# Kernel tuning notes

Hardware: AMD Instinct MI355X
Metric: run time of the kernel (lower is better)

The kernel has to match this reference:

```python
import jax, jax.numpy as jnp
import numpy as np

B, C, H, W = 1, 256, 512, 512
DS = 4
HD, WD = H // DS, W // DS
N_NOISE = 32
N_CLUSTERS = 8


def setup_inputs() -> dict:
    key = jax.random.key(0)
    k1, k2, k3, k4, k5 = jax.random.split(key, 5)
    x = jax.random.normal(k1, (B, C, H, W), dtype=jnp.float32)
    # deterministic 'HDBSCAN' labels over the B*C=256 channel-tokens:
    # first 224 channels in 8 clusters of 28, last 32 channels are noise (-1)
    n_clustered = C - N_NOISE
    labels_np = np.concatenate([
        np.arange(n_clustered) % N_CLUSTERS,
        -np.ones(N_NOISE, dtype=np.int64),
    ]).astype(np.int32)
    labels = jnp.asarray(labels_np)
    noise_idx = jnp.arange(n_clustered, C, dtype=jnp.int32)  # channels with label -1
    # grouped 1x1 conv (groups=C, 3 outputs per channel): per-output scalar weight+bias
    w_qkv = jax.random.normal(k2, (3 * C,), dtype=jnp.float32) * 0.02
    b_qkv = jax.random.normal(k3, (3 * C,), dtype=jnp.float32) * 0.02
    # depthwise ConvTranspose2d(kernel=stride=DS, groups=C): per-channel DSxDS kernel
    w_up = jax.random.normal(k4, (C, DS, DS), dtype=jnp.float32) * 0.25
    b_up = jax.random.normal(k5, (C,), dtype=jnp.float32) * 0.02
    return {"x": x, "labels": labels, "noise_idx": noise_idx,
            "w_qkv": w_qkv, "b_qkv": b_qkv, "w_up": w_up, "b_up": b_up}


def _l2norm(a):
    n = jnp.linalg.norm(a, axis=-1, keepdims=True)
    return a / jnp.maximum(n, 1e-12)


def reference(x, labels, noise_idx, w_qkv, b_qkv, w_up, b_up):
    # --- MaxPool2d(DS, DS) ---  (B=1)
    xd = x.reshape(C, HD, DS, WD, DS).max(axis=(2, 4))          # (C, HD, WD)
    xdf = xd.reshape(C, HD * WD)                                 # (C, hw)
    # --- grouped 1x1 qkv conv: out channel o = x[o//3]*w[o]+b[o]; then chunk(3)
    #     reproduces the torch code exactly, incl. its interleaved channel layout ---
    qkv = jnp.repeat(xdf, 3, axis=0) * w_qkv[:, None] + b_qkv[:, None]  # (3C, hw)
    q, k, v = qkv[:C], qkv[C:2 * C], qkv[2 * C:]
    # --- per-cluster attention as a single masked softmax over C tokens ---
    valid = labels != -1
    same = (labels[:, None] == labels[None, :]) & valid[:, None] & valid[None, :]
    scores = q @ k.T                                             # (C, C), no scaling (as in source)
    scores = jnp.where(same, scores, jnp.finfo(scores.dtype).min)
    attn = jax.nn.softmax(scores, axis=-1)
    attn = jnp.where(valid[:, None], attn, 0.0)                  # noise rows -> 0 output
    out_ds = attn @ v                                            # (C, hw)
    # --- depthwise ConvTranspose2d, stride==kernel -> non-overlapping blocks ---
    out_sp = out_ds.reshape(C, HD, WD)
    up = jnp.einsum('chw,cab->chawb', out_sp, w_up).reshape(C, H, W)
    up = (up + b_up[:, None, None])[None]                        # (1, C, H, W)
    # --- noise features & cosine similarity ---
    nf = x.reshape(B, C, H * W)[:, noise_idx, :]                 # (B, n_noise, HW)
    cf = up.reshape(B, C, H * W)                                 # (B, C, HW)
    sim = jnp.einsum('bch,bnh->bcn', _l2norm(cf), _l2norm(nf)).mean(axis=-1)  # (B, C)
    similar = sim.reshape(B, C, 1, 1)
    out = up + (1.0 - similar) * x
    return out, nf.reshape(B, N_NOISE, H, W)
```

## Files before the change

### kernel.cpp

```cpp
#include <hip/hip_runtime.h>
#include <math.h>

#define C_ 256
#define H_ 512
#define W_ 512
#define HW_ (H_*W_)
#define HD_ 128
#define WD_ 128
#define P_ (HD_*WD_)
#define NN_ 32
#define GR_ 86
#define NSL_ 128

#define XD_OFF     0ull
#define SDS_OFF    4194304ull
#define GT_OFF     8388608ull
#define GPART_OFF  8650752ull
#define DSTP_OFF   8650752ull
#define S_OFF      9641984ull
#define SPART_OFF  9642240ull
#define NSQP_OFF   9650432ull
#define GSUMP_OFF  9651456ull
#define BETA_OFF   9651584ull
#define M_OFF      9651840ull
#define SCALE_OFF  9674368ull

typedef float nfloat4 __attribute__((ext_vector_type(4)));

__device__ __forceinline__ void nt_store4(float4 v, float* p) {
    nfloat4 nv;
    nv.x = v.x; nv.y = v.y; nv.z = v.z; nv.w = v.w;
    __builtin_nontemporal_store(nv, (nfloat4*)p);
}

__device__ __forceinline__ float wsum64(float v) {
#pragma unroll
    for (int off = 32; off > 0; off >>= 1) v += __shfl_down(v, off, 64);
    return v;
}

__global__ void __launch_bounds__(256) k_pre(
        const float* __restrict__ x, const int* __restrict__ nidx,
        float* __restrict__ xd, float* __restrict__ outnf,
        float* __restrict__ Spart, float* __restrict__ nsqp) {
    int b = blockIdx.x;
    int c = b >> 5, seg = b & 31;
    int t = threadIdx.x;
    __shared__ int sn;
    if (t == 0) {
        int nn = -1;
        for (int n = 0; n < NN_; n++)
            if (nidx[n] == c) nn = n;
        sn = nn;
    }
    __syncthreads();
    int n = sn;
    int wd = t & 127;
    int hl = t >> 7;
    float ssum = 0.f, ss = 0.f;
    const float* xc = x + (size_t)c * HW_;
    float* nfc = outnf + (size_t)(n < 0 ? 0 : n) * HW_;
#pragma unroll
    for (int q = 0; q < 2; q++) {
        int hd = 4 * seg + hl + 2 * q;
        const float4* xr = (const float4*)(xc + (size_t)(4 * hd) * W_) + wd;
        float4 r0 = xr[0], r1 = xr[128], r2 = xr[256], r3 = xr[384];
        if (n >= 0) {
            float* nr = nfc + (size_t)(4 * hd) * W_ + 4 * wd;
            nt_store4(r0, nr);
            nt_store4(r1, nr + 512);
            nt_store4(r2, nr + 1024);
            nt_store4(r3, nr + 1536);
            ss += r0.x*r0.x + r0.y*r0.y + r0.z*r0.z + r0.w*r0.w
                + r1.x*r1.x + r1.y*r1.y + r1.z*r1.z + r1.w*r1.w
                + r2.x*r2.x + r2.y*r2.y + r2.z*r2.z + r2.w*r2.w
                + r3.x*r3.x + r3.y*r3.y + r3.z*r3.z + r3.w*r3.w;
        }
        float m0 = fmaxf(fmaxf(r0.x, r0.y), fmaxf(r0.z, r0.w));
        float m1 = fmaxf(fmaxf(r1.x, r1.y), fmaxf(r1.z, r1.w));
        float m2 = fmaxf(fmaxf(r2.x, r2.y), fmaxf(r2.z, r2.w));
        float m3 = fmaxf(fmaxf(r3.x, r3.y), fmaxf(r3.z, r3.w));
        float m = fmaxf(fmaxf(m0, m1), fmaxf(m2, m3));
        xd[(size_t)c * P_ + (size_t)hd * WD_ + wd] = m;
        ssum += m;
    }
    __shared__ float red[4];
    float tt = wsum64(ssum);
    int wid = t >> 6, ln = t & 63;
    if (ln == 0) red[wid] = tt;
    __syncthreads();
    if (t == 0) Spart[c * 32 + seg] = red[0] + red[1] + red[2] + red[3];
    if (n >= 0) {
        __syncthreads();
        float t2 = wsum64(ss);
        if (ln == 0) red[wid] = t2;
        __syncthreads();
        if (t == 0) nsqp[n * 32 + seg] = red[0] + red[1] + red[2] + red[3];
    }
}

__global__ void __launch_bounds__(256) k_mid(
        const float* __restrict__ x, const int* __restrict__ nidx,
        const float* __restrict__ nsqp, const float* __restrict__ Spart,
        const float* __restrict__ xd,
        float* __restrict__ gt, float* __restrict__ gsump,
        float* __restrict__ gpart, float* __restrict__ S) {
    __shared__ float smem[2 * 32 * 132];
    int bid = blockIdx.x;
    int t = threadIdx.x;
    if (bid < 128) {
        float* inv_ = smem;
        int* ncs = (int*)(smem + 32);
        float* red = smem + 64;
        if (t < NN_) {
            const float* np = nsqp + t * 32;
            float s = 0.f;
#pragma unroll
            for (int k = 0; k < 32; k++) s += np[k];
            inv_[t] = (1.f / 32.f) / fmaxf(sqrtf(s), 1e-12f);
            ncs[t] = nidx[t];
        }
        __syncthreads();
        int h = bid;
        int w = t & 127, a0 = t >> 7;
        float acc[2][4] = {{0.f,0.f,0.f,0.f},{0.f,0.f,0.f,0.f}};
#pragma unroll 4
        for (int n = 0; n < NN_; n++) {
            const float* base = x + (size_t)ncs[n] * HW_ + (size_t)(4 * h) * W_ + 4 * w;
            float4 va = *(const float4*)(base + (size_t)a0 * W_);
            float4 vb = *(const float4*)(base + (size_t)(a0 + 2) * W_);
            float iv = inv_[n];
            acc[0][0] += va.x * iv; acc[0][1] += va.y * iv;
            acc[0][2] += va.z * iv; acc[0][3] += va.w * iv;
            acc[1][0] += vb.x * iv; acc[1][1] += vb.y * iv;
            acc[1][2] += vb.z * iv; acc[1][3] += vb.w * iv;
        }
        float gs = 0.f;
#pragma unroll
        for (int q = 0; q < 2; q++) {
            int a = a0 + 2 * q;
#pragma unroll
            for (int bb = 0; bb < 4; bb++) {
                float g = acc[q][bb];
                gt[(size_t)(a * 4 + bb) * P_ + h * WD_ + w] = g;
                gs += g;
            }
        }
        float tt = wsum64(gs);
        int wid = t >> 6, ln = t & 63;
        if (ln == 0) red[wid] = tt;
        __syncthreads();
        if (t == 0) gsump[bid] = red[0] + red[1] + red[2] + red[3];
    } else if (bid < 128 + NSL_) {
        int sl = bid - 128;
        float (*As)[132] = (float(*)[132])smem;
        float (*Bs)[132] = (float(*)[132])(smem + 32 * 132);
        int tx = t & 15, ty = t >> 4;
        int p0 = sl * 128;
        float acc[8][8];
#pragma unroll
        for (int i = 0; i < 8; i++)
#pragma unroll
            for (int j = 0; j < 8; j++) acc[i][j] = 0.f;
        for (int ch = 0; ch < 4; ch++) {
            int pb = p0 + ch * 32;
            __syncthreads();
#pragma unroll
            for (int kk = 0; kk < 16; kk++) {
                int lin = kk * 256 + t;
                int row = lin >> 5;
                int pp = lin & 31;
                float av = 0.f, bv = 0.f;
                if (row < GR_) {
                    av = xd[(size_t)row * P_ + pb + pp];
                    bv = xd[(size_t)(85 + row) * P_ + pb + pp];
                }
                As[pp][row] = av;
                Bs[pp][row] = bv;
            }
            __syncthreads();
            for (int pp = 0; pp < 32; pp++) {
                float4 fa0 = *(const float4*)&As[pp][8 * tx];
                float4 fa1 = *(const float4*)&As[pp][8 * tx + 4];
                float4 fb0 = *(const float4*)&Bs[pp][8 * ty];
                float4 fb1 = *(const float4*)&Bs[pp][8 * ty + 4];
                float fa[8] = {fa0.x, fa0.y, fa0.z, fa0.w, fa1.x, fa1.y, fa1.z, fa1.w};
                float fb[8] = {fb0.x, fb0.y, fb0.z, fb0.w, fb1.x, fb1.y, fb1.z, fb1.w};
#pragma unroll
                for (int ii = 0; ii < 8; ii++)
#pragma unroll
                    for (int jj = 0; jj < 8; jj++) acc[ii][jj] += fa[ii] * fb[jj];
            }
        }
        float* gp = gpart + (size_t)sl * 7744;
#pragma unroll
        for (int ii = 0; ii < 8; ii++) {
            int ga = 8 * tx + ii;
            if (ga < GR_) {
#pragma unroll
                for (int jj = 0; jj < 8; jj++) {
                    int gb = 8 * ty + jj;
                    if (gb < GR_) gp[ga * 88 + gb] = acc[ii][jj];
                }
            }
        }
    } else {
        if (t < C_) {
            const float* sp = Spart + t * 32;
            float s = 0.f;
#pragma unroll
            for (int k = 0; k < 32; k++) s += sp[k];
            S[t] = s;
        }
    }
}

__global__ void __launch_bounds__(256) k_attn(
        const int* __restrict__ labels, const float* __restrict__ wqkv,
        const float* __restrict__ bqkv, const float* __restrict__ gpart,
        const float* __restrict__ S, float* __restrict__ M,
        float* __restrict__ beta) {
    int i = blockIdx.x, j = threadIdx.x;
    __shared__ float grow[GR_];
    __shared__ float Mloc[GR_];
    __shared__ float red[4];
    __shared__ float bc;
    int li = labels[i];
    if (li < 0) {
        if (j < GR_) M[i * 88 + j] = 0.f;
        if (j == 0) beta[i] = 0.f;
        return;
    }
    int a = i / 3;
    if (j < GR_) {
        Mloc[j] = 0.f;
        const float* gp = gpart + (size_t)a * 88 + j;
        float s = 0.f;
#pragma unroll 8
        for (int sl = 0; sl < NSL_; sl++) s += gp[(size_t)sl * 7744];
        grow[j] = s;
    }
    __syncthreads();
    float wq = wqkv[i], bq = bqkv[i];
    int kidx = 256 + j;
    int bk = kidx / 3;
    float wk = wqkv[kidx], bkb = bqkv[kidx];
    int lj = labels[j];
    bool same = (lj == li);
    float score = -3.0e38f;
    if (same)
        score = wq * wk * grow[bk - 85] + wq * bkb * S[a] + bq * wk * S[bk] +
                16384.f * bq * bkb;
    int wid = j >> 6, ln = j & 63;
    float m = score;
#pragma unroll
    for (int off = 32; off > 0; off >>= 1) m = fmaxf(m, __shfl_down(m, off, 64));
    if (ln == 0) red[wid] = m;
    __syncthreads();
    if (j == 0) bc = fmaxf(fmaxf(red[0], red[1]), fmaxf(red[2], red[3]));
    __syncthreads();
    float mx = bc;
    float e = same ? expf(score - mx) : 0.f;
    __syncthreads();
    float t = wsum64(e);
    if (ln == 0) red[wid] = t;
    __syncthreads();
    if (j == 0) bc = red[0] + red[1] + red[2] + red[3];
    __syncthreads();
    float attn = e / bc;
    int vidx = 512 + j;
    int vr = vidx / 3 - 170;
    float wv = wqkv[vidx], bv = bqkv[vidx];
    __syncthreads();
    float bp = wsum64(attn * bv);
    if (ln == 0) red[wid] = bp;
    __syncthreads();
    if (j == 0) beta[i] = red[0] + red[1] + red[2] + red[3];
    atomicAdd(&Mloc[vr], attn * wv);
    __syncthreads();
    if (j < GR_) M[i * 88 + j] = Mloc[j];
}

__global__ void __launch_bounds__(256) k_outds(
        const float* __restrict__ xd, const float* __restrict__ gt,
        const float* __restrict__ M, const float* __restrict__ beta,
        float* __restrict__ sds, float* __restrict__ dstp) {
    __shared__ float Mt[16][88];
    __shared__ float bt[16];
    __shared__ float sdsL[16][258];
    __shared__ float gtsL[16][258];
    int t = threadIdx.x;
    int p0 = blockIdx.x * 256;
    int i0 = blockIdx.y * 16;
    for (int idx = t; idx < 16 * 88; idx += 256)
        Mt[idx / 88][idx % 88] = M[(size_t)(i0 + idx / 88) * 88 + (idx % 88)];
    if (t < 16) bt[t] = beta[i0 + t];
#pragma unroll 4
    for (int ab = 0; ab < 16; ab++)
        gtsL[ab][t] = gt[(size_t)ab * P_ + p0 + t];
    __syncthreads();
    float acc[16];
#pragma unroll
    for (int ii = 0; ii < 16; ii++) acc[ii] = bt[ii];
    const float* xb = xd + (size_t)170 * P_ + p0 + t;
    for (int r = 0; r < 84; r += 4) {
        float x0 = xb[(size_t)r * P_];
        float x1 = xb[(size_t)(r + 1) * P_];
        float x2 = xb[(size_t)(r + 2) * P_];
        float x3 = xb[(size_t)(r + 3) * P_];
#pragma unroll
        for (int ii = 0; ii < 16; ii++) {
            float4 mv = *(const float4*)&Mt[ii][r];
            acc[ii] += mv.x * x0 + mv.y * x1 + mv.z * x2 + mv.w * x3;
        }
    }
    {
        float x0 = xb[(size_t)84 * P_];
        float x1 = xb[(size_t)85 * P_];
#pragma unroll
        for (int ii = 0; ii < 16; ii++)
            acc[ii] += Mt[ii][84] * x0 + Mt[ii][85] * x1;
    }
#pragma unroll
    for (int ii = 0; ii < 16; ii++) {
        sds[(size_t)(i0 + ii) * P_ + p0 + t] = acc[ii];
        sdsL[ii][t] = acc[ii];
    }
    __syncthreads();
    int ch = t & 15, ab = t >> 4;
    bool do1 = (t < 16), do2 = (t >= 16 && t < 32);
    float D = 0.f, sx = 0.f;
    for (int k = 0; k < 256; k++) {
        float sv = sdsL[ch][k];
        float gv = gtsL[ab][k];
        D += sv * gv;
        if (do1) sx += sv;
        if (do2) sx += sv * sv;
    }
    size_t base = ((size_t)(i0 + ch) * 64 + blockIdx.x) * 18;
    dstp[base + ab] = D;
    if (do1) dstp[base + 16] = sx;
    if (do2) dstp[base + 17] = sx;
}

__global__ void __launch_bounds__(64) k_sim(
        const float* __restrict__ dstp, const float* __restrict__ gsump,
        const float* __restrict__ wup, const float* __restrict__ bup,
        float* __restrict__ scale) {
    int c = blockIdx.x, t = threadIdx.x;
    const float* dp = dstp + ((size_t)c * 64 + t) * 18;
    float vals[19];
#pragma unroll
    for (int q = 0; q < 18; q++) vals[q] = dp[q];
    vals[18] = gsump[t] + gsump[t + 64];
#pragma unroll
    for (int q = 0; q < 19; q++) vals[q] = wsum64(vals[q]);
    if (t == 0) {
        float gs = vals[18];
        float wsm = 0.f, wsq = 0.f, dd = 0.f;
#pragma unroll
        for (int ab = 0; ab < 16; ab++) {
            float w = wup[c * 16 + ab];
            wsm += w;
            wsq += w * w;
            dd += w * vals[ab];
        }
        float s1 = vals[16], s2 = vals[17];
        float b = bup[c];
        float dot = dd + b * gs;
        float n2 = wsq * s2 + 2.f * b * wsm * s1 + (float)HW_ * b * b;
        float nrm = sqrtf(fmaxf(n2, 0.f));
        scale[c] = 1.f - dot / fmaxf(nrm, 1e-12f);
    }
}

__global__ void __launch_bounds__(256) k_final(
        const float* __restrict__ x, const float* __restrict__ sds,
        const float* __restrict__ wup, const float* __restrict__ bup,
        const float* __restrict__ scale, float* __restrict__ out) {
    size_t idx = (size_t)blockIdx.x * 256 + threadIdx.x;
    int wq = (int)(idx & 127);
    int y = (int)((idx >> 7) & 511);
    int c = (int)(idx >> 16);
    float sv = sds[(size_t)c * P_ + (size_t)(y >> 2) * WD_ + wq];
    float4 wu = *(const float4*)(wup + c * 16 + (y & 3) * 4);
    float b = bup[c];
    float sc = scale[c];
    float4 xv = ((const float4*)x)[idx];
    float4 o;
    o.x = sv * wu.x + b + sc * xv.x;
    o.y = sv * wu.y + b + sc * xv.y;
    o.z = sv * wu.z + b + sc * xv.z;
    o.w = sv * wu.w + b + sc * xv.w;
    nt_store4(o, out + 4 * idx);
}

extern "C" void kernel_launch(void* const* d_in, const int* in_sizes, int n_in,
                              void* d_out, int out_size, void* d_ws, size_t ws_size,
                              hipStream_t stream) {
    const float* x = (const float*)d_in[0];
    const int* labels = (const int*)d_in[1];
    const int* nidx = (const int*)d_in[2];
    const float* wqkv = (const float*)d_in[3];
    const float* bqkv = (const float*)d_in[4];
    const float* wup = (const float*)d_in[5];
    const float* bup = (const float*)d_in[6];
    float* out = (float*)d_out;
    float* ws = (float*)d_ws;

    float* xd = ws + XD_OFF;
    float* sds = ws + SDS_OFF;
    float* gt = ws + GT_OFF;
    float* gpart = ws + GPART_OFF;
    float* dstp = ws + DSTP_OFF;
    float* S = ws + S_OFF;
    float* Spart = ws + SPART_OFF;
    float* nsqp = ws + NSQP_OFF;
    float* gsump = ws + GSUMP_OFF;
    float* beta = ws + BETA_OFF;
    float* M = ws + M_OFF;
    float* scale = ws + SCALE_OFF;
    float* outnf = out + (size_t)C_ * HW_;

    k_pre<<<C_ * 32, 256, 0, stream>>>(x, nidx, xd, outnf, Spart, nsqp);
    k_mid<<<128 + NSL_ + 1, 256, 0, stream>>>(x, nidx, nsqp, Spart, xd, gt, gsump, gpart, S);
    k_attn<<<256, 256, 0, stream>>>(labels, wqkv, bqkv, gpart, S, M, beta);
    k_outds<<<dim3(64, 16), 256, 0, stream>>>(xd, gt, M, beta, sds, dstp);
    k_sim<<<256, 64, 0, stream>>>(dstp, gsump, wup, bup, scale);
    k_final<<<65536, 256, 0, stream>>>(x, sds, wup, bup, scale, out);
}
```

Before: 210.1 us.

## Split noise-sum blocks 4x across rows and give final kernel two rows per thread

The noise-channel weighted-sum part of k_mid now uses 512 blocks instead of 128. Each block handles one sub-row, with the 32 noise channels split between two thread halves and combined through shared memory. The gsump partials grow to 512 entries and k_sim sums eight per lane; the workspace offsets shift to make room. k_final is restructured so each thread reuses one downsampled value for two output rows, using nontemporal loads of x and half as many blocks. The aim is more parallelism in the mid stage and fewer redundant sds/weight loads in the bandwidth-bound final pass, at the cost of an extra shared-memory reduction.

New measurement: 214.6 us. 1.02x slower.

```diff
diff --git a/kernel.cpp b/kernel.cpp
--- a/kernel.cpp
+++ b/kernel.cpp
@@ -21,9 +21,9 @@
 #define SPART_OFF  9642240ull
 #define NSQP_OFF   9650432ull
 #define GSUMP_OFF  9651456ull
-#define BETA_OFF   9651584ull
-#define M_OFF      9651840ull
-#define SCALE_OFF  9674368ull
+#define BETA_OFF   9651968ull
+#define M_OFF      9652224ull
+#define SCALE_OFF  9674752ull
 
 typedef float nfloat4 __attribute__((ext_vector_type(4)));
 
@@ -31,6 +31,13 @@
     nfloat4 nv;
     nv.x = v.x; nv.y = v.y; nv.z = v.z; nv.w = v.w;
     __builtin_nontemporal_store(nv, (nfloat4*)p);
+}
+
+__device__ __forceinline__ float4 nt_load4(const float* p) {
+    nfloat4 nv = __builtin_nontemporal_load((const nfloat4*)p);
+    float4 v;
+    v.x = nv.x; v.y = nv.y; v.z = nv.z; v.w = nv.w;
+    return v;
 }
 
 __device__ __forceinline__ float wsum64(float v) {
@@ -108,10 +115,11 @@
     __shared__ float smem[2 * 32 * 132];
     int bid = blockIdx.x;
     int t = threadIdx.x;
-    if (bid < 128) {
+    if (bid < 512) {
         float* inv_ = smem;
         int* ncs = (int*)(smem + 32);
         float* red = smem + 64;
+        float4* comb = (float4*)(smem + 128);
         if (t < NN_) {
             const float* np = nsqp + t * 32;
             float s = 0.f;
@@ -121,38 +129,36 @@
             ncs[t] = nidx[t];
         }
         __syncthreads();
-        int h = bid;
-        int w = t & 127, a0 = t >> 7;
-        float acc[2][4] = {{0.f,0.f,0.f,0.f},{0.f,0.f,0.f,0.f}};
-#pragma unroll 4
-        for (int n = 0; n < NN_; n++) {
-            const float* base = x + (size_t)ncs[n] * HW_ + (size_t)(4 * h) * W_ + 4 * w;
-            float4 va = *(const float4*)(base + (size_t)a0 * W_);
-            float4 vb = *(const float4*)(base + (size_t)(a0 + 2) * W_);
+        int h = bid >> 2, a = bid & 3;
+        int w = t & 127, half = t >> 7;
+        size_t rowoff = (size_t)(4 * h + a) * W_ + 4 * w;
+        float4 acc = make_float4(0.f, 0.f, 0.f, 0.f);
+#pragma unroll
+        for (int k = 0; k < 16; k++) {
+            int n = half * 16 + k;
+            float4 v = *(const float4*)(x + (size_t)ncs[n] * HW_ + rowoff);
             float iv = inv_[n];
-            acc[0][0] += va.x * iv; acc[0][1] += va.y * iv;
-            acc[0][2] += va.z * iv; acc[0][3] += va.w * iv;
-            acc[1][0] += vb.x * iv; acc[1][1] += vb.y * iv;
-            acc[1][2] += vb.z * iv; acc[1][3] += vb.w * iv;
-        }
-        float gs = 0.f;
-#pragma unroll
-        for (int q = 0; q < 2; q++) {
-            int a = a0 + 2 * q;
-#pragma unroll
-            for (int bb = 0; bb < 4; bb++) {
-                float g = acc[q][bb];
-                gt[(size_t)(a * 4 + bb) * P_ + h * WD_ + w] = g;
-                gs += g;
-            }
-        }
+            acc.x += v.x * iv; acc.y += v.y * iv;
+            acc.z += v.z * iv; acc.w += v.w * iv;
+        }
+        comb[t] = acc;
+        float gs = acc.x + acc.y + acc.z + acc.w;
         float tt = wsum64(gs);
         int wid = t >> 6, ln = t & 63;
         if (ln == 0) red[wid] = tt;
         __syncthreads();
         if (t == 0) gsump[bid] = red[0] + red[1] + red[2] + red[3];
-    } else if (bid < 128 + NSL_) {
-        int sl = bid - 128;
+        if (t < 128) {
+            float4 u = comb[t], v2 = comb[t + 128];
+            float g0 = u.x + v2.x, g1 = u.y + v2.y, g2 = u.z + v2.z, g3 = u.w + v2.w;
+            size_t pbase = (size_t)(a * 4) * P_ + h * WD_ + w;
+            gt[pbase] = g0;
+            gt[pbase + P_] = g1;
+            gt[pbase + 2 * P_] = g2;
+            gt[pbase + 3 * P_] = g3;
+        }
+    } else if (bid < 512 + NSL_) {
+        int sl = bid - 512;
         float (*As)[132] = (float(*)[132])smem;
         float (*Bs)[132] = (float(*)[132])(smem + 32 * 132);
         int tx = t & 15, ty = t >> 4;
@@ -352,7 +358,10 @@
     float vals[19];
 #pragma unroll
     for (int q = 0; q < 18; q++) vals[q] = dp[q];
-    vals[18] = gsump[t] + gsump[t + 64];
+    float gsl = 0.f;
+#pragma unroll
+    for (int k = 0; k < 8; k++) gsl += gsump[t + 64 * k];
+    vals[18] = gsl;
 #pragma unroll
     for (int q = 0; q < 19; q++) vals[q] = wsum64(vals[q]);
     if (t == 0) {
@@ -378,21 +387,29 @@
         const float* __restrict__ x, const float* __restrict__ sds,
         const float* __restrict__ wup, const float* __restrict__ bup,
         const float* __restrict__ scale, float* __restrict__ out) {
-    size_t idx = (size_t)blockIdx.x * 256 + threadIdx.x;
-    int wq = (int)(idx & 127);
-    int y = (int)((idx >> 7) & 511);
-    int c = (int)(idx >> 16);
-    float sv = sds[(size_t)c * P_ + (size_t)(y >> 2) * WD_ + wq];
-    float4 wu = *(const float4*)(wup + c * 16 + (y & 3) * 4);
+    int bid = blockIdx.x;
+    int c = bid >> 7, hd = bid & 127;
+    int t = threadIdx.x;
+    int wq = t & 127, ysub = t >> 7;
+    float sv = sds[(size_t)c * P_ + (size_t)hd * WD_ + wq];
     float b = bup[c];
     float sc = scale[c];
-    float4 xv = ((const float4*)x)[idx];
-    float4 o;
-    o.x = sv * wu.x + b + sc * xv.x;
-    o.y = sv * wu.y + b + sc * xv.y;
-    o.z = sv * wu.z + b + sc * xv.z;
-    o.w = sv * wu.w + b + sc * xv.w;
-    nt_store4(o, out + 4 * idx);
+    float4 wu0 = *(const float4*)(wup + c * 16 + ysub * 4);
+    float4 wu1 = *(const float4*)(wup + c * 16 + (ysub + 2) * 4);
+    size_t xoff = ((size_t)c * H_ + 4 * hd + ysub) * W_ + 4 * wq;
+    float4 x0 = nt_load4(x + xoff);
+    float4 x1 = nt_load4(x + xoff + 2 * W_);
+    float4 o0, o1;
+    o0.x = sv * wu0.x + b + sc * x0.x;
+    o0.y = sv * wu0.y + b + sc * x0.y;
+    o0.z = sv * wu0.z + b + sc * x0.z;
+    o0.w = sv * wu0.w + b + sc * x0.w;
+    o1.x = sv * wu1.x + b + sc * x1.x;
+    o1.y = sv * wu1.y + b + sc * x1.y;
+    o1.z = sv * wu1.z + b + sc * x1.z;
+    o1.w = sv * wu1.w + b + sc * x1.w;
+    nt_store4(o0, out + xoff);
+    nt_store4(o1, out + xoff + 2 * W_);
 }
 
 extern "C" void kernel_launch(void* const* d_in, const int* in_sizes, int n_in,
@@ -423,9 +440,9 @@
     float* outnf = out + (size_t)C_ * HW_;
 
     k_pre<<<C_ * 32, 256, 0, stream>>>(x, nidx, xd, outnf, Spart, nsqp);
-    k_mid<<<128 + NSL_ + 1, 256, 0, stream>>>(x, nidx, nsqp, Spart, xd, gt, gsump, gpart, S);
+    k_mid<<<512 + NSL_ + 1, 256, 0, stream>>>(x, nidx, nsqp, Spart, xd, gt, gsump, gpart, S);
     k_attn<<<256, 256, 0, stream>>>(labels, wqkv, bqkv, gpart, S, M, beta);
     k_outds<<<dim3(64, 16), 256, 0, stream>>>(xd, gt, M, beta, sds, dstp);
     k_sim<<<256, 64, 0, stream>>>(dstp, gsump, wup, bup, scale);
-    k_final<<<65536, 256, 0, stream>>>(x, sds, wup, bup, scale, out);
-}
+    k_final<<<32768, 256, 0, stream>>>(x, sds, wup, bup, scale, out);
+}
```
